# Performance work log

Measured on AMD Instinct MI355X. Metric: run time of the kernel, lower is better.

The kernel has to match this reference:

```python
import jax, jax.numpy as jnp
import numpy as np

EPSILON = 1e-05


def setup_inputs() -> dict:
    key = jax.random.key(0)
    X = jax.random.normal(key, (4, 2048, 3), dtype=jnp.float32)
    K = jnp.ones((), dtype=jnp.float32)
    B = jnp.zeros((), dtype=jnp.float32)
    return {"X": X, "K": K, "B": B}


def reference(X, K, B):
    # X: [batch, N, D]
    delta_X = X[:, :, None, :] - X[:, None, :, :]          # [b, N, N, D]
    sq = jnp.sum(delta_X * delta_X, axis=-1, keepdims=True)  # [b, N, N, 1]
    # safe sqrt: distance is 0 on the diagonal; avoid nan-producing grad paths
    distance = jnp.sqrt(jnp.where(sq == 0, 1.0, sq))
    distance = jnp.where(sq == 0, 0.0, distance)
    direction = delta_X / (distance + EPSILON)
    force = (K * (distance - B)) * direction               # [b, N, N, D]
    aggregated_force = jnp.sum(force, axis=-2)             # [b, N, D]
    return X + aggregated_force
```

## Files before the change

kernel.cpp:

```cpp
#include <hip/hip_runtime.h>

#define NPTS 2048
#define EPSF 1e-5f

__global__ __launch_bounds__(256) void spring_kernel(
    const float* __restrict__ X,
    const float* __restrict__ Kp,
    const float* __restrict__ Bp,
    float* __restrict__ out)
{
    __shared__ __align__(16) float xs[NPTS];
    __shared__ __align__(16) float ys[NPTS];
    __shared__ __align__(16) float zs[NPTS];

    const int tid    = threadIdx.x;
    const int b      = blockIdx.x >> 7;
    const int i_base = (blockIdx.x & 127) << 4;
    const float* Xb  = X + b * (NPTS * 3);

    for (int e = tid; e < NPTS * 3; e += 256) {
        float v = Xb[e];
        int n = e / 3;
        int c = e - n * 3;
        if (c == 0)      xs[n] = v;
        else if (c == 1) ys[n] = v;
        else             zs[n] = v;
    }
    __syncthreads();

    const float K  = Kp[0];
    const float KB = K * Bp[0];

    const int il = tid >> 4;
    const int js = tid & 15;
    const int i  = i_base + il;

    const float xi = xs[i], yi = ys[i], zi = zs[i];

    const float4* xs4 = (const float4*)xs;
    const float4* ys4 = (const float4*)ys;
    const float4* zs4 = (const float4*)zs;

    float ax = 0.f, ay = 0.f, az = 0.f;

    #pragma unroll 4
    for (int t = 0; t < NPTS / 4 / 16; ++t) {
        const int idx = t * 16 + js;
        float4 jx = xs4[idx];
        float4 jy = ys4[idx];
        float4 jz = zs4[idx];

        #define PAIR(cx, cy, cz)                                   \
        {                                                          \
            float dx = xi - (cx), dy = yi - (cy), dz = zi - (cz);  \
            float sq = fmaf(dx, dx, fmaf(dy, dy, dz * dz));        \
            sq = fmaxf(sq, 1e-30f);      \
            float r = __builtin_amdgcn_rsqf(sq);                   \
            float s = fmaf(-KB, r, K);              \
            ax = fmaf(dx, s, ax);                                  \
            ay = fmaf(dy, s, ay);                                  \
            az = fmaf(dz, s, az);                                  \
        }
        PAIR(jx.x, jy.x, jz.x)
        PAIR(jx.y, jy.y, jz.y)
        PAIR(jx.z, jy.z, jz.z)
        PAIR(jx.w, jy.w, jz.w)
        #undef PAIR
    }

    for (int d = 8; d > 0; d >>= 1) {
        ax += __shfl_down(ax, d, 16);
        ay += __shfl_down(ay, d, 16);
        az += __shfl_down(az, d, 16);
    }

    if (js == 0) {
        float* o = out + (b * NPTS + i) * 3;
        o[0] = xi + ax;
        o[1] = yi + ay;
        o[2] = zi + az;
    }
}

extern "C" void kernel_launch(void* const* d_in, const int* in_sizes, int n_in,
                              void* d_out, int out_size, void* d_ws, size_t ws_size,
                              hipStream_t stream) {
    const float* X  = (const float*)d_in[0];
    const float* Kp = (const float*)d_in[1];
    const float* Bp = (const float*)d_in[2];
    float* out = (float*)d_out;

    dim3 grid(4 * (NPTS / 16));
    dim3 block(256);
    spring_kernel<<<grid, block, 0, stream>>>(X, Kp, Bp, out);
}
```

Before: 66.99 us.

## Register-block four target points per thread to reuse shared-memory loads

Reassigns work so each wavefront owns four i-points and each lane accumulates forces for all four. Each loaded float4 of j-coordinates is reused across the four points. This cuts LDS loads per interaction fourfold. In exchange it uses more registers and needs a full 64-lane shuffle reduction for twelve accumulators.

```diff
diff --git a/kernel.cpp b/kernel.cpp
--- a/kernel.cpp
+++ b/kernel.cpp
@@ -1,7 +1,6 @@
 #include <hip/hip_runtime.h>
 
 #define NPTS 2048
-#define EPSF 1e-5f
 
 __global__ __launch_bounds__(256) void spring_kernel(
     const float* __restrict__ X,
@@ -31,54 +30,69 @@
     const float K  = Kp[0];
     const float KB = K * Bp[0];
 
-    const int il = tid >> 4;
-    const int js = tid & 15;
-    const int i  = i_base + il;
+    const int wv   = tid >> 6;
+    const int lane = tid & 63;
+    const int i0   = i_base + wv * 4;
 
-    const float xi = xs[i], yi = ys[i], zi = zs[i];
+    float xi[4], yi[4], zi[4];
+    float ax[4] = {0.f,0.f,0.f,0.f};
+    float ay[4] = {0.f,0.f,0.f,0.f};
+    float az[4] = {0.f,0.f,0.f,0.f};
+    #pragma unroll
+    for (int q = 0; q < 4; ++q) {
+        xi[q] = xs[i0 + q]; yi[q] = ys[i0 + q]; zi[q] = zs[i0 + q];
+    }
 
     const float4* xs4 = (const float4*)xs;
     const float4* ys4 = (const float4*)ys;
     const float4* zs4 = (const float4*)zs;
 
-    float ax = 0.f, ay = 0.f, az = 0.f;
-
-    #pragma unroll 4
-    for (int t = 0; t < NPTS / 4 / 16; ++t) {
-        const int idx = t * 16 + js;
+    #pragma unroll 2
+    for (int t = 0; t < NPTS / 4 / 64; ++t) {
+        const int idx = t * 64 + lane;
         float4 jx = xs4[idx];
         float4 jy = ys4[idx];
         float4 jz = zs4[idx];
+        const float jxa[4] = {jx.x, jx.y, jx.z, jx.w};
+        const float jya[4] = {jy.x, jy.y, jy.z, jy.w};
+        const float jza[4] = {jz.x, jz.y, jz.z, jz.w};
 
-        #define PAIR(cx, cy, cz)                                   \
-        {                                                          \
-            float dx = xi - (cx), dy = yi - (cy), dz = zi - (cz);  \
-            float sq = fmaf(dx, dx, fmaf(dy, dy, dz * dz));        \
-            sq = fmaxf(sq, 1e-30f);      \
-            float r = __builtin_amdgcn_rsqf(sq);                   \
-            float s = fmaf(-KB, r, K);              \
-            ax = fmaf(dx, s, ax);                                  \
-            ay = fmaf(dy, s, ay);                                  \
-            az = fmaf(dz, s, az);                                  \
+        #pragma unroll
+        for (int c = 0; c < 4; ++c) {
+            #pragma unroll
+            for (int q = 0; q < 4; ++q) {
+                float dx = xi[q] - jxa[c];
+                float dy = yi[q] - jya[c];
+                float dz = zi[q] - jza[c];
+                float sq = fmaf(dx, dx, fmaf(dy, dy, dz * dz));
+                sq = fmaxf(sq, 1e-30f);
+                float r = __builtin_amdgcn_rsqf(sq);
+                float s = fmaf(-KB, r, K);
+                ax[q] = fmaf(dx, s, ax[q]);
+                ay[q] = fmaf(dy, s, ay[q]);
+                az[q] = fmaf(dz, s, az[q]);
+            }
         }
-        PAIR(jx.x, jy.x, jz.x)
-        PAIR(jx.y, jy.y, jz.y)
-        PAIR(jx.z, jy.z, jz.z)
-        PAIR(jx.w, jy.w, jz.w)
-        #undef PAIR
     }
 
-    for (int d = 8; d > 0; d >>= 1) {
-        ax += __shfl_down(ax, d, 16);
-        ay += __shfl_down(ay, d, 16);
-        az += __shfl_down(az, d, 16);
+    #pragma unroll
+    for (int q = 0; q < 4; ++q) {
+        #pragma unroll
+        for (int d = 32; d > 0; d >>= 1) {
+            ax[q] += __shfl_down(ax[q], d, 64);
+            ay[q] += __shfl_down(ay[q], d, 64);
+            az[q] += __shfl_down(az[q], d, 64);
+        }
     }
 
-    if (js == 0) {
-        float* o = out + (b * NPTS + i) * 3;
-        o[0] = xi + ax;
-        o[1] = yi + ay;
-        o[2] = zi + az;
+    if (lane == 0) {
+        #pragma unroll
+        for (int q = 0; q < 4; ++q) {
+            float* o = out + (b * NPTS + i0 + q) * 3;
+            o[0] = xi[q] + ax[q];
+            o[1] = yi[q] + ay[q];
+            o[2] = zi[q] + az[q];
+        }
     }
 }
 
```

Result: no change. 65.69 us (-2.0%).
